# Kernel tuning notes

Measured on AMD Instinct MI355X. Metric: run time of the kernel, lower is better.

Reference implementation:

```python
import math
import jax, jax.numpy as jnp
import numpy as np

S, M, B, D, H = 256, 256, 8, 512, 8
HD = D // H
K = S + M  # key_len


def setup_inputs() -> dict:
    key = jax.random.key(0)
    ks = jax.random.split(key, 10)
    x = jax.random.normal(ks[0], (S, B, D), jnp.float32)
    memory = jax.random.normal(ks[1], (M, B, D), jnp.float32)
    rel_pos = jax.random.normal(ks[2], (K, D), jnp.float32)
    # causal mask: True means masked (key position after query position)
    q_pos = jnp.arange(S)[:, None] + M  # (S,1)
    k_pos = jnp.arange(K)[None, :]     # (1,K)
    attn_mask = jnp.broadcast_to(k_pos > q_pos, (B, S, K))
    scale = 1.0 / math.sqrt(D)
    Wq = jax.random.normal(ks[3], (D, D), jnp.float32) * scale
    Wk = jax.random.normal(ks[4], (D, D), jnp.float32) * scale
    Wv = jax.random.normal(ks[5], (D, D), jnp.float32) * scale
    Wr = jax.random.normal(ks[6], (D, D), jnp.float32) * scale
    Wo = jax.random.normal(ks[7], (D, D), jnp.float32) * scale
    u_bias = jax.random.normal(ks[8], (H, HD), jnp.float32) * 0.02
    v_bias = jax.random.normal(ks[9], (H, HD), jnp.float32) * 0.02
    return {"x": x, "memory": memory, "rel_pos": rel_pos, "attn_mask": attn_mask,
            "Wq": Wq, "Wk": Wk, "Wv": Wv, "Wr": Wr, "Wo": Wo,
            "u_bias": u_bias, "v_bias": v_bias}


def reference(x, memory, rel_pos, attn_mask, Wq, Wk, Wv, Wr, Wo, u_bias, v_bias):
    mem = jax.lax.stop_gradient(memory)
    kv = jnp.concatenate([mem, x], axis=0)  # (K, B, D)
    # projections (torch Linear: y = x @ W.T)
    q = (x @ Wq.T).reshape(S, B, H, HD).transpose(1, 2, 0, 3)   # (B,H,S,HD)
    k = (kv @ Wk.T).reshape(K, B, H, HD).transpose(1, 2, 0, 3)  # (B,H,K,HD)
    v = (kv @ Wv.T).reshape(K, B, H, HD).transpose(1, 2, 0, 3)  # (B,H,K,HD)
    r = (rel_pos[:K] @ Wr.T).reshape(K, H, HD)                  # (K,H,HD)
    # relative index gather
    q_pos = jnp.arange(S)[:, None] + M
    k_pos = jnp.arange(K)[None, :]
    rel_idx = jnp.clip(q_pos - k_pos, 0, K - 1)  # (S,K)
    r_qk = r[rel_idx]                            # (S,K,H,HD)
    qk = jnp.einsum('bhqd,bhkd->bhqk', q, k)
    qr = jnp.einsum('bhqd,qkhd->bhqk', q, r_qk)
    uk = jnp.einsum('hd,bhkd->bhk', u_bias, k)[:, :, None, :]
    vr = jnp.einsum('hd,qkhd->hqk', v_bias, r_qk)[None]
    scores = (qk + qr + uk + vr) / math.sqrt(HD)  # (B,H,S,K)
    scores = jnp.where(attn_mask[:, None, :, :], -jnp.inf, scores)
    weights = jax.nn.softmax(scores, axis=-1)
    y = jnp.einsum('bhqk,bhkd->bhqd', weights, v)
    y = y.transpose(2, 0, 1, 3).reshape(S, B, D)
    return y @ Wo.T
```

## Files before the change

kernel.cpp:

```cpp
#include <hip/hip_runtime.h>
#include <math.h>

constexpr int S_  = 256;
constexpr int Mm  = 256;
constexpr int Bb  = 8;
constexpr int Dd  = 512;
constexpr int Hh  = 8;
constexpr int HDd = 64;
constexpr int Kk  = 512;

typedef unsigned short u16;
typedef short bf16x8 __attribute__((ext_vector_type(8)));
typedef float f32x4  __attribute__((ext_vector_type(4)));

constexpr int LROW = 72;
constexpr int QSTR = 520;

__device__ __forceinline__ u16 f2b(float f) {
  union { float f; unsigned int u; } v; v.f = f;
  unsigned int u = v.u + 0x7fffu + ((v.u >> 16) & 1u);
  return (u16)(u >> 16);
}
__device__ __forceinline__ float b2f(u16 b) {
  union { unsigned int u; float f; } v; v.u = ((unsigned int)b) << 16;
  return v.f;
}

__device__ __forceinline__ void stage_bf16(u16* dst, const u16* __restrict__ src,
                                           int ld, int tid) {
  const int r = tid >> 3, c = (tid & 7) * 8;
  *(int4*)(dst + r * LROW + c)        = *(const int4*)(src + (size_t)r * ld + c);
  *(int4*)(dst + (r + 32) * LROW + c) = *(const int4*)(src + (size_t)(r + 32) * ld + c);
}
__device__ __forceinline__ void stage_f32(u16* dst, const float* __restrict__ src,
                                          int ld, int tid) {
  const int r = tid >> 3, c = (tid & 7) * 8;
#pragma unroll
  for (int hh = 0; hh < 2; ++hh) {
    const float4 a = *(const float4*)(src + (size_t)(r + 32 * hh) * ld + c);
    const float4 b = *(const float4*)(src + (size_t)(r + 32 * hh) * ld + c + 4);
    union { u16 u[8]; int4 v; } p;
    p.u[0] = f2b(a.x); p.u[1] = f2b(a.y); p.u[2] = f2b(a.z); p.u[3] = f2b(a.w);
    p.u[4] = f2b(b.x); p.u[5] = f2b(b.y); p.u[6] = f2b(b.z); p.u[7] = f2b(b.w);
    *(int4*)(dst + (r + 32 * hh) * LROW + c) = p.v;
  }
}

__device__ __forceinline__ void mfma_step(const u16* As, const u16* Bs,
                                          f32x4 (&acc)[4], int wave, int lane) {
  const int r16 = lane & 15, q8 = (lane >> 4) * 8;
#pragma unroll
  for (int ks = 0; ks < 64; ks += 32) {
    const bf16x8 a = *(const bf16x8*)(As + (wave * 16 + r16) * LROW + ks + q8);
#pragma unroll
    for (int nb = 0; nb < 4; ++nb) {
      const bf16x8 b = *(const bf16x8*)(Bs + (nb * 16 + r16) * LROW + ks + q8);
      acc[nb] = __builtin_amdgcn_mfma_f32_16x16x32_bf16(a, b, acc[nb], 0, 0, 0);
    }
  }
}

__global__ __launch_bounds__(256) void k_proj(const float* __restrict__ x,
                                              const float* __restrict__ mem,
                                              const float* __restrict__ rel,
                                              const float* __restrict__ Wq,
                                              const float* __restrict__ Wk,
                                              const float* __restrict__ Wv,
                                              const float* __restrict__ Wr,
                                              const float* __restrict__ ub,
                                              const float* __restrict__ vb,
                                              u16* __restrict__ qu,
                                              u16* __restrict__ qv,
                                              u16* __restrict__ kb,
                                              u16* __restrict__ vT,
                                              u16* __restrict__ rT) {
  __shared__ u16 As[64 * LROW], Bs[64 * LROW];
  const int tid = threadIdx.x, wave = tid >> 6, lane = tid & 63;
  const int bid = blockIdx.x;
  int kind, n0, m0;
  const float *A, *B;
  if (bid < 256)       { kind = 0; int t = bid;        n0 = (t & 7) * 64; m0 = (t >> 3) * 64; A = x + (size_t)m0 * Dd; B = Wq; }
  else if (bid < 768)  { kind = 1; int t = bid - 256;  n0 = (t & 7) * 64; m0 = (t >> 3) * 64;
                         A = (m0 < Mm * Bb) ? mem + (size_t)m0 * Dd : x + (size_t)(m0 - Mm * Bb) * Dd; B = Wk; }
  else if (bid < 1280) { kind = 2; int t = bid - 768;  n0 = (t & 7) * 64; m0 = (t >> 3) * 64;
                         A = (m0 < Mm * Bb) ? mem + (size_t)m0 * Dd : x + (size_t)(m0 - Mm * Bb) * Dd; B = Wv; }
  else                 { kind = 3; int t = bid - 1280; n0 = (t & 7) * 64; m0 = (t >> 3) * 64; A = rel + (size_t)m0 * Dd; B = Wr; }
  B += (size_t)n0 * Dd;

  f32x4 acc[4];
#pragma unroll
  for (int i = 0; i < 4; ++i) acc[i] = (f32x4){0.f, 0.f, 0.f, 0.f};
  for (int k0 = 0; k0 < Dd; k0 += 64) {
    stage_f32(As, A + k0, Dd, tid);
    stage_f32(Bs, B + k0, Dd, tid);
    __syncthreads();
    mfma_step(As, Bs, acc, wave, lane);
    __syncthreads();
  }

  const int col = lane & 15, rq = (lane >> 4) * 4;
  if (kind == 0) {
#pragma unroll
    for (int nb = 0; nb < 4; ++nb) {
      const int n = n0 + nb * 16 + col;
      const int h = n >> 6, hd = n & 63;
      const float u = ub[n], v = vb[n];
#pragma unroll
      for (int r = 0; r < 4; ++r) {
        const int m = m0 + wave * 16 + rq + r;
        const int s = m >> 3, b = m & 7;
        const size_t d = ((size_t)(b * Hh + h) * S_ + s) * HDd + hd;
        qu[d] = f2b(acc[nb][r] + u);
        qv[d] = f2b(acc[nb][r] + v);
      }
    }
  } else if (kind == 1) {
#pragma unroll
    for (int nb = 0; nb < 4; ++nb) {
      const int n = n0 + nb * 16 + col;
      const int h = n >> 6, hd = n & 63;
#pragma unroll
      for (int r = 0; r < 4; ++r) {
        const int m = m0 + wave * 16 + rq + r;
        const int pos = m >> 3, b = m & 7;
        kb[((size_t)(b * Hh + h) * Kk + pos) * HDd + hd] = f2b(acc[nb][r]);
      }
    }
  } else if (kind == 2) {
#pragma unroll
    for (int nb = 0; nb < 4; ++nb) {
      const int n = n0 + nb * 16 + col;
      const int h = n >> 6, hd = n & 63;
#pragma unroll
      for (int r = 0; r < 4; ++r) {
        const int m = m0 + wave * 16 + rq + r;
        const int pos = m >> 3, b = m & 7;
        vT[((size_t)(b * Hh + h) * HDd + hd) * Kk + pos] = f2b(acc[nb][r]);
      }
    }
  } else {
#pragma unroll
    for (int nb = 0; nb < 4; ++nb) {
      const int n = n0 + nb * 16 + col;
      const int h = n >> 6, hd = n & 63;
#pragma unroll
      for (int r = 0; r < 4; ++r) {
        const int j = m0 + wave * 16 + rq + r;
        rT[((size_t)h * Kk + j) * HDd + hd] = f2b(acc[nb][r]);
      }
    }
  }
}

__global__ __launch_bounds__(256) void k_attn(const u16* __restrict__ qu,
                                              const u16* __restrict__ qv,
                                              const u16* __restrict__ kb,
                                              const u16* __restrict__ vT,
                                              const u16* __restrict__ rT,
                                              u16* __restrict__ y) {
  extern __shared__ u16 lds[];
  u16* QRP = lds;
  u16* As  = lds + 64 * QSTR;
  u16* Bs  = As + 64 * LROW;
  const int tid = threadIdx.x, wave = tid >> 6, lane = tid & 63;
  const int q0 = blockIdx.x * 64, bh = blockIdx.y, h = bh & 7, b = bh >> 3;
  const int ntiles = (q0 >> 6) + 5;
  const int col = lane & 15, rq = (lane >> 4) * 4;
  const int r16 = lane & 15, q8 = (lane >> 4) * 8;

  stage_bf16(As, qv + ((size_t)bh * S_ + q0) * HDd, HDd, tid);
#pragma unroll
  for (int jt = 0; jt < 8; ++jt) if (jt < ntiles) {
    stage_bf16(Bs, rT + ((size_t)h * Kk + jt * 64) * HDd, HDd, tid);
    __syncthreads();
    f32x4 c[4];
#pragma unroll
    for (int i = 0; i < 4; ++i) c[i] = (f32x4){0.f, 0.f, 0.f, 0.f};
    mfma_step(As, Bs, c, wave, lane);
#pragma unroll
    for (int nb = 0; nb < 4; ++nb)
#pragma unroll
      for (int r = 0; r < 4; ++r)
        QRP[(wave * 16 + rq + r) * QSTR + jt * 64 + nb * 16 + col] = f2b(c[nb][r]);
    __syncthreads();
  }

  stage_bf16(As, qu + ((size_t)bh * S_ + q0) * HDd, HDd, tid);
  f32x4 sc[8][4];
#pragma unroll
  for (int kt = 0; kt < 8; ++kt) if (kt < ntiles) {
    stage_bf16(Bs, kb + ((size_t)bh * Kk + kt * 64) * HDd, HDd, tid);
    __syncthreads();
#pragma unroll
    for (int i = 0; i < 4; ++i) sc[kt][i] = (f32x4){0.f, 0.f, 0.f, 0.f};
    mfma_step(As, Bs, sc[kt], wave, lane);
    __syncthreads();
  }

  float mx[4] = {-INFINITY, -INFINITY, -INFINITY, -INFINITY};
#pragma unroll
  for (int kt = 0; kt < 8; ++kt) if (kt < ntiles) {
#pragma unroll
    for (int nb = 0; nb < 4; ++nb) {
      const int kk = kt * 64 + nb * 16 + col;
#pragma unroll
      for (int r = 0; r < 4; ++r) {
        const int ql = wave * 16 + rq + r;
        const int q  = q0 + ql;
        float v;
        if (kk <= q + Mm) {
          const float qr = b2f(QRP[ql * QSTR + (q + Mm - kk)]);
          v = (sc[kt][nb][r] + qr) * 0.125f;
        } else {
          v = -INFINITY;
        }
        sc[kt][nb][r] = v;
        mx[r] = fmaxf(mx[r], v);
      }
    }
  }
#pragma unroll
  for (int r = 0; r < 4; ++r)
#pragma unroll
    for (int off = 1; off < 16; off <<= 1) mx[r] = fmaxf(mx[r], __shfl_xor(mx[r], off));
  float sum[4] = {0.f, 0.f, 0.f, 0.f};
#pragma unroll
  for (int kt = 0; kt < 8; ++kt) if (kt < ntiles)
#pragma unroll
    for (int nb = 0; nb < 4; ++nb)
#pragma unroll
      for (int r = 0; r < 4; ++r) {
        const float p = __expf(sc[kt][nb][r] - mx[r]);
        sc[kt][nb][r] = p;
        sum[r] += p;
      }
#pragma unroll
  for (int r = 0; r < 4; ++r)
#pragma unroll
    for (int off = 1; off < 16; off <<= 1) sum[r] += __shfl_xor(sum[r], off);
  float inv[4];
#pragma unroll
  for (int r = 0; r < 4; ++r) inv[r] = 1.0f / sum[r];

#pragma unroll
  for (int kt = 0; kt < 8; ++kt) if (kt < ntiles)
#pragma unroll
    for (int nb = 0; nb < 4; ++nb)
#pragma unroll
      for (int r = 0; r < 4; ++r)
        QRP[(wave * 16 + rq + r) * QSTR + kt * 64 + nb * 16 + col] =
            f2b(sc[kt][nb][r] * inv[r]);
  __syncthreads();

  f32x4 o[4];
#pragma unroll
  for (int i = 0; i < 4; ++i) o[i] = (f32x4){0.f, 0.f, 0.f, 0.f};
#pragma unroll
  for (int kt = 0; kt < 8; ++kt) if (kt < ntiles) {
    stage_bf16(Bs, vT + (size_t)bh * HDd * Kk + kt * 64, Kk, tid);
    __syncthreads();
#pragma unroll
    for (int ks = 0; ks < 64; ks += 32) {
      const bf16x8 a = *(const bf16x8*)(QRP + (wave * 16 + r16) * QSTR + kt * 64 + ks + q8);
#pragma unroll
      for (int nb = 0; nb < 4; ++nb) {
        const bf16x8 bv = *(const bf16x8*)(Bs + (nb * 16 + r16) * LROW + ks + q8);
        o[nb] = __builtin_amdgcn_mfma_f32_16x16x32_bf16(a, bv, o[nb], 0, 0, 0);
      }
    }
    __syncthreads();
  }
#pragma unroll
  for (int nb = 0; nb < 4; ++nb) {
    const int hd = nb * 16 + col;
#pragma unroll
    for (int r = 0; r < 4; ++r) {
      const int q = q0 + wave * 16 + rq + r;
      y[((size_t)q * Bb + b) * Dd + h * HDd + hd] = f2b(o[nb][r]);
    }
  }
}

__global__ __launch_bounds__(256) void k_out(const u16* __restrict__ y,
                                             const float* __restrict__ Wo,
                                             float* __restrict__ out) {
  __shared__ u16 As[64 * LROW], Bs[64 * LROW];
  const int tid = threadIdx.x, wave = tid >> 6, lane = tid & 63;
  const int n0 = blockIdx.x * 64, m0 = blockIdx.y * 64;
  f32x4 acc[4];
#pragma unroll
  for (int i = 0; i < 4; ++i) acc[i] = (f32x4){0.f, 0.f, 0.f, 0.f};
  for (int k0 = 0; k0 < Dd; k0 += 64) {
    stage_bf16(As, y + (size_t)m0 * Dd + k0, Dd, tid);
    stage_f32(Bs, Wo + (size_t)n0 * Dd + k0, Dd, tid);
    __syncthreads();
    mfma_step(As, Bs, acc, wave, lane);
    __syncthreads();
  }
  const int col = lane & 15, rq = (lane >> 4) * 4;
#pragma unroll
  for (int nb = 0; nb < 4; ++nb) {
    const int n = n0 + nb * 16 + col;
#pragma unroll
    for (int r = 0; r < 4; ++r) {
      const int m = m0 + wave * 16 + rq + r;
      out[(size_t)m * Dd + n] = acc[nb][r];
    }
  }
}

extern "C" void kernel_launch(void* const* d_in, const int* in_sizes, int n_in,
                              void* d_out, int out_size, void* d_ws, size_t ws_size,
                              hipStream_t stream) {
  const float* x    = (const float*)d_in[0];
  const float* mem  = (const float*)d_in[1];
  const float* rel  = (const float*)d_in[2];
  const float* Wq = (const float*)d_in[4];
  const float* Wk = (const float*)d_in[5];
  const float* Wv = (const float*)d_in[6];
  const float* Wr = (const float*)d_in[7];
  const float* Wo = (const float*)d_in[8];
  const float* ub = (const float*)d_in[9];
  const float* vb = (const float*)d_in[10];
  float* out = (float*)d_out;

  u16* qu = (u16*)d_ws;
  u16* qv = qu + 1048576;
  u16* kb = qv + 1048576;
  u16* vT = kb + 2097152;
  u16* rT = vT + 2097152;
  u16* yb = rT + 262144;

  constexpr int ATTN_LDS = (64 * QSTR + 2 * 64 * LROW) * (int)sizeof(u16);
  (void)hipFuncSetAttribute((const void*)k_attn,
                            hipFuncAttributeMaxDynamicSharedMemorySize, ATTN_LDS);

  k_proj<<<dim3(1344),   dim3(256), 0,        stream>>>(x, mem, rel, Wq, Wk, Wv, Wr,
                                                        ub, vb, qu, qv, kb, vT, rT);
  k_attn<<<dim3(4, 64),  dim3(256), ATTN_LDS, stream>>>(qu, qv, kb, vT, rT, yb);
  k_out <<<dim3(8, 32),  dim3(256), 0,        stream>>>(yb, Wo, out);
}
```

Baseline: 149.8 us.

## Use 128-row tiles in projection GEMM and keep Q fragments in registers

The projection kernel now computes 128x64 output tiles, with each wave owning two 16-row MFMA sub-tiles. This halves the block count and reuses each staged weight tile across twice as many rows, cutting redundant fp32 weight loads and conversions. In the attention kernel the Q fragments (qu, qv) are loaded straight from global memory into registers instead of being staged through LDS, which frees LDS and drops a staging step. The cost is more accumulator registers per thread in k_proj and fewer blocks to fill the GPU.

```diff
diff --git a/kernel.cpp b/kernel.cpp
--- a/kernel.cpp
+++ b/kernel.cpp
@@ -33,10 +33,9 @@
   *(int4*)(dst + (r + 32) * LROW + c) = *(const int4*)(src + (size_t)(r + 32) * ld + c);
 }
 __device__ __forceinline__ void stage_f32(u16* dst, const float* __restrict__ src,
-                                          int ld, int tid) {
+                                          int ld, int tid, int nrow32) {
   const int r = tid >> 3, c = (tid & 7) * 8;
-#pragma unroll
-  for (int hh = 0; hh < 2; ++hh) {
+  for (int hh = 0; hh < nrow32; ++hh) {
     const float4 a = *(const float4*)(src + (size_t)(r + 32 * hh) * ld + c);
     const float4 b = *(const float4*)(src + (size_t)(r + 32 * hh) * ld + c + 4);
     union { u16 u[8]; int4 v; } p;
@@ -74,80 +73,104 @@
                                               u16* __restrict__ kb,
                                               u16* __restrict__ vT,
                                               u16* __restrict__ rT) {
-  __shared__ u16 As[64 * LROW], Bs[64 * LROW];
+  __shared__ u16 As[128 * LROW], Bs[64 * LROW];
   const int tid = threadIdx.x, wave = tid >> 6, lane = tid & 63;
+  const int r16 = lane & 15, q8 = (lane >> 4) * 8, rq = (lane >> 4) * 4;
   const int bid = blockIdx.x;
-  int kind, n0, m0;
+  int kind, mt, nt;
   const float *A, *B;
-  if (bid < 256)       { kind = 0; int t = bid;        n0 = (t & 7) * 64; m0 = (t >> 3) * 64; A = x + (size_t)m0 * Dd; B = Wq; }
-  else if (bid < 768)  { kind = 1; int t = bid - 256;  n0 = (t & 7) * 64; m0 = (t >> 3) * 64;
-                         A = (m0 < Mm * Bb) ? mem + (size_t)m0 * Dd : x + (size_t)(m0 - Mm * Bb) * Dd; B = Wk; }
-  else if (bid < 1280) { kind = 2; int t = bid - 768;  n0 = (t & 7) * 64; m0 = (t >> 3) * 64;
-                         A = (m0 < Mm * Bb) ? mem + (size_t)m0 * Dd : x + (size_t)(m0 - Mm * Bb) * Dd; B = Wv; }
-  else                 { kind = 3; int t = bid - 1280; n0 = (t & 7) * 64; m0 = (t >> 3) * 64; A = rel + (size_t)m0 * Dd; B = Wr; }
+  if (bid < 128)      { kind = 0; int t = bid;       mt = t >> 3; nt = t & 7; B = Wq; }
+  else if (bid < 384) { kind = 1; int t = bid - 128; mt = t >> 3; nt = t & 7; B = Wk; }
+  else if (bid < 640) { kind = 2; int t = bid - 384; mt = t >> 3; nt = t & 7; B = Wv; }
+  else                { kind = 3; int t = bid - 640; mt = t >> 3; nt = t & 7; B = Wr; }
+  const int m0 = mt * 128, n0 = nt * 64;
+  if (kind == 0)      A = x + (size_t)m0 * Dd;
+  else if (kind == 3) A = rel + (size_t)m0 * Dd;
+  else                A = (m0 < Mm * Bb) ? mem + (size_t)m0 * Dd
+                                         : x + (size_t)(m0 - Mm * Bb) * Dd;
   B += (size_t)n0 * Dd;
 
-  f32x4 acc[4];
-#pragma unroll
-  for (int i = 0; i < 4; ++i) acc[i] = (f32x4){0.f, 0.f, 0.f, 0.f};
+  f32x4 acc[2][4];
+#pragma unroll
+  for (int mi = 0; mi < 2; ++mi)
+#pragma unroll
+    for (int nb = 0; nb < 4; ++nb) acc[mi][nb] = (f32x4){0.f, 0.f, 0.f, 0.f};
+
   for (int k0 = 0; k0 < Dd; k0 += 64) {
-    stage_f32(As, A + k0, Dd, tid);
-    stage_f32(Bs, B + k0, Dd, tid);
-    __syncthreads();
-    mfma_step(As, Bs, acc, wave, lane);
-    __syncthreads();
-  }
-
-  const int col = lane & 15, rq = (lane >> 4) * 4;
+    stage_f32(As, A + k0, Dd, tid, 4);
+    stage_f32(Bs, B + k0, Dd, tid, 2);
+    __syncthreads();
+#pragma unroll
+    for (int ks = 0; ks < 64; ks += 32) {
+      bf16x8 a[2];
+#pragma unroll
+      for (int mi = 0; mi < 2; ++mi)
+        a[mi] = *(const bf16x8*)(As + (wave * 32 + mi * 16 + r16) * LROW + ks + q8);
+#pragma unroll
+      for (int nb = 0; nb < 4; ++nb) {
+        const bf16x8 bb = *(const bf16x8*)(Bs + (nb * 16 + r16) * LROW + ks + q8);
+#pragma unroll
+        for (int mi = 0; mi < 2; ++mi)
+          acc[mi][nb] = __builtin_amdgcn_mfma_f32_16x16x32_bf16(a[mi], bb, acc[mi][nb], 0, 0, 0);
+      }
+    }
+    __syncthreads();
+  }
+
+  const int h = n0 >> 6;
   if (kind == 0) {
 #pragma unroll
     for (int nb = 0; nb < 4; ++nb) {
-      const int n = n0 + nb * 16 + col;
-      const int h = n >> 6, hd = n & 63;
+      const int hd = nb * 16 + r16, n = n0 + hd;
       const float u = ub[n], v = vb[n];
 #pragma unroll
-      for (int r = 0; r < 4; ++r) {
-        const int m = m0 + wave * 16 + rq + r;
-        const int s = m >> 3, b = m & 7;
-        const size_t d = ((size_t)(b * Hh + h) * S_ + s) * HDd + hd;
-        qu[d] = f2b(acc[nb][r] + u);
-        qv[d] = f2b(acc[nb][r] + v);
-      }
+      for (int mi = 0; mi < 2; ++mi)
+#pragma unroll
+        for (int r = 0; r < 4; ++r) {
+          const int m = m0 + wave * 32 + mi * 16 + rq + r;
+          const int s = m >> 3, b = m & 7;
+          const size_t d = ((size_t)(b * Hh + h) * S_ + s) * HDd + hd;
+          qu[d] = f2b(acc[mi][nb][r] + u);
+          qv[d] = f2b(acc[mi][nb][r] + v);
+        }
     }
   } else if (kind == 1) {
 #pragma unroll
     for (int nb = 0; nb < 4; ++nb) {
-      const int n = n0 + nb * 16 + col;
-      const int h = n >> 6, hd = n & 63;
-#pragma unroll
-      for (int r = 0; r < 4; ++r) {
-        const int m = m0 + wave * 16 + rq + r;
-        const int pos = m >> 3, b = m & 7;
-        kb[((size_t)(b * Hh + h) * Kk + pos) * HDd + hd] = f2b(acc[nb][r]);
-      }
+      const int hd = nb * 16 + r16;
+#pragma unroll
+      for (int mi = 0; mi < 2; ++mi)
+#pragma unroll
+        for (int r = 0; r < 4; ++r) {
+          const int m = m0 + wave * 32 + mi * 16 + rq + r;
+          const int pos = m >> 3, b = m & 7;
+          kb[((size_t)(b * Hh + h) * Kk + pos) * HDd + hd] = f2b(acc[mi][nb][r]);
+        }
     }
   } else if (kind == 2) {
 #pragma unroll
     for (int nb = 0; nb < 4; ++nb) {
-      const int n = n0 + nb * 16 + col;
-      const int h = n >> 6, hd = n & 63;
-#pragma unroll
-      for (int r = 0; r < 4; ++r) {
-        const int m = m0 + wave * 16 + rq + r;
-        const int pos = m >> 3, b = m & 7;
-        vT[((size_t)(b * Hh + h) * HDd + hd) * Kk + pos] = f2b(acc[nb][r]);
-      }
+      const int hd = nb * 16 + r16;
+#pragma unroll
+      for (int mi = 0; mi < 2; ++mi)
+#pragma unroll
+        for (int r = 0; r < 4; ++r) {
+          const int m = m0 + wave * 32 + mi * 16 + rq + r;
+          const int pos = m >> 3, b = m & 7;
+          vT[((size_t)(b * Hh + h) * HDd + hd) * Kk + pos] = f2b(acc[mi][nb][r]);
+        }
     }
   } else {
 #pragma unroll
     for (int nb = 0; nb < 4; ++nb) {
-      const int n = n0 + nb * 16 + col;
-      const int h = n >> 6, hd = n & 63;
-#pragma unroll
-      for (int r = 0; r < 4; ++r) {
-        const int j = m0 + wave * 16 + rq + r;
-        rT[((size_t)h * Kk + j) * HDd + hd] = f2b(acc[nb][r]);
-      }
+      const int hd = nb * 16 + r16;
+#pragma unroll
+      for (int mi = 0; mi < 2; ++mi)
+#pragma unroll
+        for (int r = 0; r < 4; ++r) {
+          const int j = m0 + wave * 32 + mi * 16 + rq + r;
+          rT[((size_t)h * Kk + j) * HDd + hd] = f2b(acc[mi][nb][r]);
+        }
     }
   }
 }
@@ -160,15 +183,16 @@
                                               u16* __restrict__ y) {
   extern __shared__ u16 lds[];
   u16* QRP = lds;
-  u16* As  = lds + 64 * QSTR;
-  u16* Bs  = As + 64 * LROW;
+  u16* Bs  = lds + 64 * QSTR;
   const int tid = threadIdx.x, wave = tid >> 6, lane = tid & 63;
   const int q0 = blockIdx.x * 64, bh = blockIdx.y, h = bh & 7, b = bh >> 3;
   const int ntiles = (q0 >> 6) + 5;
   const int col = lane & 15, rq = (lane >> 4) * 4;
   const int r16 = lane & 15, q8 = (lane >> 4) * 8;
 
-  stage_bf16(As, qv + ((size_t)bh * S_ + q0) * HDd, HDd, tid);
+  const u16* qvp = qv + ((size_t)bh * S_ + q0 + wave * 16 + r16) * HDd;
+  const bf16x8 av0 = *(const bf16x8*)(qvp + q8);
+  const bf16x8 av1 = *(const bf16x8*)(qvp + 32 + q8);
 #pragma unroll
   for (int jt = 0; jt < 8; ++jt) if (jt < ntiles) {
     stage_bf16(Bs, rT + ((size_t)h * Kk + jt * 64) * HDd, HDd, tid);
@@ -176,7 +200,15 @@
     f32x4 c[4];
 #pragma unroll
     for (int i = 0; i < 4; ++i) c[i] = (f32x4){0.f, 0.f, 0.f, 0.f};
-    mfma_step(As, Bs, c, wave, lane);
+#pragma unroll
+    for (int ks = 0; ks < 64; ks += 32) {
+      const bf16x8 a = ks ? av1 : av0;
+#pragma unroll
+      for (int nb = 0; nb < 4; ++nb) {
+        const bf16x8 bb = *(const bf16x8*)(Bs + (nb * 16 + r16) * LROW + ks + q8);
+        c[nb] = __builtin_amdgcn_mfma_f32_16x16x32_bf16(a, bb, c[nb], 0, 0, 0);
+      }
+    }
 #pragma unroll
     for (int nb = 0; nb < 4; ++nb)
 #pragma unroll
@@ -185,7 +217,9 @@
     __syncthreads();
   }
 
-  stage_bf16(As, qu + ((size_t)bh * S_ + q0) * HDd, HDd, tid);
+  const u16* qup = qu + ((size_t)bh * S_ + q0 + wave * 16 + r16) * HDd;
+  const bf16x8 au0 = *(const bf16x8*)(qup + q8);
+  const bf16x8 au1 = *(const bf16x8*)(qup + 32 + q8);
   f32x4 sc[8][4];
 #pragma unroll
   for (int kt = 0; kt < 8; ++kt) if (kt < ntiles) {
@@ -193,7 +227,15 @@
     __syncthreads();
 #pragma unroll
     for (int i = 0; i < 4; ++i) sc[kt][i] = (f32x4){0.f, 0.f, 0.f, 0.f};
-    mfma_step(As, Bs, sc[kt], wave, lane);
+#pragma unroll
+    for (int ks = 0; ks < 64; ks += 32) {
+      const bf16x8 a = ks ? au1 : au0;
+#pragma unroll
+      for (int nb = 0; nb < 4; ++nb) {
+        const bf16x8 bb = *(const bf16x8*)(Bs + (nb * 16 + r16) * LROW + ks + q8);
+        sc[kt][nb] = __builtin_amdgcn_mfma_f32_16x16x32_bf16(a, bb, sc[kt][nb], 0, 0, 0);
+      }
+    }
     __syncthreads();
   }
 
@@ -292,7 +334,7 @@
   for (int i = 0; i < 4; ++i) acc[i] = (f32x4){0.f, 0.f, 0.f, 0.f};
   for (int k0 = 0; k0 < Dd; k0 += 64) {
     stage_bf16(As, y + (size_t)m0 * Dd + k0, Dd, tid);
-    stage_f32(Bs, Wo + (size_t)n0 * Dd + k0, Dd, tid);
+    stage_f32(Bs, Wo + (size_t)n0 * Dd + k0, Dd, tid, 2);
     __syncthreads();
     mfma_step(As, Bs, acc, wave, lane);
     __syncthreads();
@@ -331,12 +373,12 @@
   u16* rT = vT + 2097152;
   u16* yb = rT + 262144;
 
-  constexpr int ATTN_LDS = (64 * QSTR + 2 * 64 * LROW) * (int)sizeof(u16);
+  constexpr int ATTN_LDS = (64 * QSTR + 64 * LROW) * (int)sizeof(u16);
   (void)hipFuncSetAttribute((const void*)k_attn,
                             hipFuncAttributeMaxDynamicSharedMemorySize, ATTN_LDS);
 
-  k_proj<<<dim3(1344),   dim3(256), 0,        stream>>>(x, mem, rel, Wq, Wk, Wv, Wr,
-                                                        ub, vb, qu, qv, kb, vT, rT);
-  k_attn<<<dim3(4, 64),  dim3(256), ATTN_LDS, stream>>>(qu, qv, kb, vT, rT, yb);
-  k_out <<<dim3(8, 32),  dim3(256), 0,        stream>>>(yb, Wo, out);
-}
+  k_proj<<<dim3(672),   dim3(256), 0,        stream>>>(x, mem, rel, Wq, Wk, Wv, Wr,
+                                                       ub, vb, qu, qv, kb, vT, rT);
+  k_attn<<<dim3(4, 64), dim3(256), ATTN_LDS, stream>>>(qu, qv, kb, vT, rT, yb);
+  k_out <<<dim3(8, 32), dim3(256), 0,        stream>>>(yb, Wo, out);
+}
```

After: 149.9 us. About the same (+0.0%).
